# Optimization experiments

Measured on AMD Instinct MI355X. Metric: run time of the kernel, lower is better.

Reference implementation:

```python
import jax, jax.numpy as jnp
from jax import lax
import numpy as np

EPS = 1e-3  # keras BatchNormalization default epsilon

def _bn(x, g, b, m, v):
    return (x - m) / jnp.sqrt(v + EPS) * g + b

def _conv_relu(x, w, b):
    y = lax.conv_general_dilated(x, w, (1, 1), 'SAME', dimension_numbers=('NHWC', 'HWIO', 'NHWC'))
    return jax.nn.relu(y + b)

def _pool(x):
    return lax.reduce_window(x, -jnp.inf, lax.max, (1, 2, 2, 1), (1, 2, 2, 1), 'VALID')

def setup_inputs():
    key = jax.random.key(0)
    ks = jax.random.split(key, 24)
    B, E = 2048, 16
    rn = lambda k, s, sc=0.05: jax.random.normal(k, s, jnp.float32) * sc
    pos = lambda k, s: jax.random.uniform(k, s, jnp.float32, 0.5, 1.5)
    inp = {}
    inp['x'] = jax.random.normal(ks[0], (B, 32, 32, 3), jnp.float32)
    inp['cW1'] = rn(ks[1], (3, 3, 3, 32), 0.2); inp['cb1'] = jnp.zeros((32,), jnp.float32)
    inp['bn1g'] = pos(ks[2], (32,)); inp['bn1b'] = rn(ks[3], (32,))
    inp['bn1m'] = rn(ks[4], (32,)); inp['bn1v'] = pos(ks[5], (32,))
    inp['cW2'] = rn(ks[6], (3, 3, 32, 64), 0.1); inp['cb2'] = jnp.zeros((64,), jnp.float32)
    inp['bn2g'] = pos(ks[7], (64,)); inp['bn2b'] = rn(ks[8], (64,))
    inp['bn2m'] = rn(ks[9], (64,)); inp['bn2v'] = pos(ks[10], (64,))
    inp['dW'] = rn(ks[11], (4096, 128), 0.02); inp['db'] = jnp.zeros((128,), jnp.float32)
    inp['rW1'] = rn(ks[12], (128, 64), 0.1); inp['rb1'] = jnp.zeros((64,), jnp.float32)
    inp['rW2'] = rn(ks[13], (64, E), 0.1); inp['rb2'] = jnp.zeros((E,), jnp.float32)
    inp['eW1'] = rn(ks[14], (E, 128, 128), 0.1); inp['eb1'] = jnp.zeros((E, 128), jnp.float32)
    inp['ebng'] = pos(ks[15], (E, 128)); inp['ebnb'] = rn(ks[16], (E, 128))
    inp['ebnm'] = rn(ks[17], (E, 128)); inp['ebnv'] = pos(ks[18], (E, 128))
    inp['eW2'] = rn(ks[19], (E, 128, 64), 0.1); inp['eb2'] = jnp.zeros((E, 64), jnp.float32)
    inp['eW3'] = rn(ks[20], (E, 64, 10), 0.1); inp['eb3'] = jnp.zeros((E, 10), jnp.float32)
    return inp

def reference(x, cW1, cb1, bn1g, bn1b, bn1m, bn1v, cW2, cb2, bn2g, bn2b, bn2m, bn2v,
              dW, db, rW1, rb1, rW2, rb2, eW1, eb1, ebng, ebnb, ebnm, ebnv, eW2, eb2, eW3, eb3):
    # shared trunk: conv(relu) -> BN -> maxpool, twice; flatten; dense(relu). Dropout = identity (inference).
    h = _pool(_bn(_conv_relu(x, cW1, cb1), bn1g, bn1b, bn1m, bn1v))   # [B,16,16,32]
    h = _pool(_bn(_conv_relu(h, cW2, cb2), bn2g, bn2b, bn2m, bn2v))   # [B,8,8,64]
    feats = jax.nn.relu(h.reshape(h.shape[0], -1) @ dW + db)          # [B,128]
    # router softmax over expert logits
    router_logits = jax.nn.relu(feats @ rW1 + rb1) @ rW2 + rb2        # [B,E]
    router_probs = jax.nn.softmax(router_logits, axis=-1)
    # all experts fused into batched GEMMs over stacked weights: [E,B,*]
    e = jax.nn.relu(jnp.einsum('bd,edh->ebh', feats, eW1) + eb1[:, None, :])
    e = _bn(e, ebng[:, None, :], ebnb[:, None, :], ebnm[:, None, :], ebnv[:, None, :])
    e = jax.nn.relu(jnp.einsum('ebh,ehk->ebk', e, eW2) + eb2[:, None, :])
    e = jnp.einsum('ebk,ekc->ebc', e, eW3) + eb3[:, None, :]          # [E,B,10]
    # weighted sum combine: sum_e probs[b,e] * logits[e,b,c]
    return jnp.einsum('ebc,be->bc', e, router_probs)
```

## Files before the change

kernel.cpp:

```cpp
#include <hip/hip_runtime.h>

#define EPS 1e-3f

typedef _Float16 half8 __attribute__((ext_vector_type(8)));
typedef _Float16 half4v __attribute__((ext_vector_type(4)));
typedef float f32x4 __attribute__((ext_vector_type(4)));

__global__ __launch_bounds__(256) void k_wprep_all(
    const float* __restrict__ dW,  _Float16* __restrict__ Wt2,
    const float* __restrict__ eW1, _Float16* __restrict__ eW1t,
    const float* __restrict__ eW2, _Float16* __restrict__ eW2t,
    const float* __restrict__ cW1, _Float16* __restrict__ Wt1,
    const float* __restrict__ cW2, _Float16* __restrict__ Wt,
    const float* __restrict__ eW3, _Float16* __restrict__ eW3p)
{
    __shared__ _Float16 lsbuf[16640];
    int bx = blockIdx.x, tid = threadIdx.x;

    if (bx < 64) {
        auto lt = (_Float16(*)[137])lsbuf;
        int kb = bx * 64;
        int c = tid & 127, r2 = tid >> 7;
#pragma unroll
        for (int it = 0; it < 32; ++it) {
            int r = it * 2 + r2;
            lt[r][c] = (_Float16)dW[(long)(kb + r) * 128 + c];
        }
        __syncthreads();
#pragma unroll
        for (int it = 0; it < 4; ++it) {
            int chunk = it * 256 + tid;
            int n = chunk >> 3, kc = (chunk & 7) * 8;
            half8 v;
#pragma unroll
            for (int j = 0; j < 8; ++j) v[j] = lt[kc + j][n];
            *(half8*)(Wt2 + (long)n * 4096 + kb + kc) = v;
        }
    } else if (bx < 80) {
        auto lt = (_Float16(*)[130])lsbuf;
        int e = bx - 64;
        const float* src = eW1 + (long)e * 16384;
#pragma unroll
        for (int it = 0; it < 64; ++it) {
            int idx = it * 256 + tid;
            lt[idx >> 7][idx & 127] = (_Float16)src[idx];
        }
        __syncthreads();
        _Float16* dst = eW1t + (long)e * 16384;
#pragma unroll
        for (int it = 0; it < 64; ++it) {
            int idx = it * 256 + tid;
            dst[idx] = lt[idx & 127][idx >> 7];
        }
    } else if (bx < 96) {
        auto lt = (_Float16(*)[66])lsbuf;
        int e = bx - 80;
        const float* src = eW2 + (long)e * 8192;
#pragma unroll
        for (int it = 0; it < 32; ++it) {
            int idx = it * 256 + tid;
            lt[idx >> 6][idx & 63] = (_Float16)src[idx];
        }
        __syncthreads();
        _Float16* dst = eW2t + (long)e * 8192;
#pragma unroll
        for (int it = 0; it < 32; ++it) {
            int idx = it * 256 + tid;
            dst[idx] = lt[idx & 127][idx >> 7];
        }
    } else {
        int t = (bx - 96) * 256 + tid;
        if (t < 3072) {
            int k = t & 31, co = (t >> 5) & 31, ky = t >> 10;
            int kx = k >> 2, ci = k & 3;
            float val = (kx < 3 && ci < 3) ? cW1[((ky * 3 + kx) * 3 + ci) * 32 + co] : 0.f;
            Wt1[t] = (_Float16)val;
        } else if (t < 3072 + 18432) {
            int u = t - 3072;
            int co = u & 63;
            int rest = u >> 6;
            int ci = rest & 31, tap = rest >> 5;
            Wt[(tap * 64 + co) * 32 + ci] = (_Float16)cW2[u];
        } else if (t < 3072 + 18432 + 16384) {
            int u = t - 21504;
            int k = u & 63, n = (u >> 6) & 15, e = u >> 10;
            float val = (n < 10) ? eW3[(e * 64 + k) * 10 + n] : 0.f;
            eW3p[(e * 16 + n) * 64 + k] = (_Float16)val;
        }
    }
}

__global__ __launch_bounds__(256) void k_conv12(
    const float* __restrict__ x, const _Float16* __restrict__ Wt1,
    const float* __restrict__ b1, const float* __restrict__ g1,
    const float* __restrict__ bb1, const float* __restrict__ m1,
    const float* __restrict__ v1,
    const _Float16* __restrict__ Wt,
    const float* __restrict__ b2, const float* __restrict__ g2,
    const float* __restrict__ bb2, const float* __restrict__ m2,
    const float* __restrict__ v2,
    _Float16* __restrict__ out)
{
    __shared__ __align__(16) _Float16 As1[34][40][4];
    __shared__ __align__(16) _Float16 As2[18][18][40];
    int tid = threadIdx.x;
    int b = blockIdx.x;
    int w = tid >> 6, l = tid & 63;
    int l15 = l & 15, lq = l >> 4;

    {
        float4 z = make_float4(0.f, 0.f, 0.f, 0.f);
        float4* f1p = (float4*)&As1[0][0][0];
        for (int i = tid; i < 680; i += 256) f1p[i] = z;
        float4* f2p = (float4*)&As2[0][0][0];
        for (int i = tid; i < 1620; i += 256) f2p[i] = z;
    }
    __syncthreads();

    {
        int y = tid >> 3, x0 = (tid & 7) * 4;
        const float* src = x + ((long)b * 1024 + y * 32 + x0) * 3;
        float4 f0 = *(const float4*)(src);
        float4 f1 = *(const float4*)(src + 4);
        float4 f2 = *(const float4*)(src + 8);
        half4v h0 = { (_Float16)f0.x, (_Float16)f0.y, (_Float16)f0.z, (_Float16)0.f };
        half4v h1 = { (_Float16)f0.w, (_Float16)f1.x, (_Float16)f1.y, (_Float16)0.f };
        half4v h2 = { (_Float16)f1.z, (_Float16)f1.w, (_Float16)f2.x, (_Float16)0.f };
        half4v h3 = { (_Float16)f2.y, (_Float16)f2.z, (_Float16)f2.w, (_Float16)0.f };
        *(half4v*)&As1[y + 1][x0 + 1][0] = h0;
        *(half4v*)&As1[y + 1][x0 + 2][0] = h1;
        *(half4v*)&As1[y + 1][x0 + 3][0] = h2;
        *(half4v*)&As1[y + 1][x0 + 4][0] = h3;
    }

    half8 bf1[3][2];
#pragma unroll
    for (int ky = 0; ky < 3; ++ky)
#pragma unroll
        for (int nf = 0; nf < 2; ++nf)
            bf1[ky][nf] = *(const half8*)(Wt1 + (ky * 32 + nf * 16 + l15) * 32 + lq * 8);

    float bv1[2], gg1[2], iv1[2], mm1[2], bbv1[2];
#pragma unroll
    for (int nf = 0; nf < 2; ++nf) {
        int co = nf * 16 + l15;
        bv1[nf] = b1[co]; gg1[nf] = g1[co]; bbv1[nf] = bb1[co]; mm1[nf] = m1[co];
        iv1[nf] = rsqrtf(v1[co] + EPS);
    }
    __syncthreads();

    {
        int y0 = w * 8;
#pragma unroll
        for (int pr = 0; pr < 4; ++pr) {
            int ya = y0 + 2 * pr;
            f32x4 acc[2][2][2];
#pragma unroll
            for (int r = 0; r < 2; ++r)
#pragma unroll
                for (int h = 0; h < 2; ++h)
#pragma unroll
                    for (int nf = 0; nf < 2; ++nf)
                        acc[r][h][nf] = (f32x4){ bv1[nf], bv1[nf], bv1[nf], bv1[nf] };

#pragma unroll
            for (int ky = 0; ky < 3; ++ky)
#pragma unroll
                for (int r = 0; r < 2; ++r)
#pragma unroll
                    for (int h = 0; h < 2; ++h) {
                        const _Float16* ap = &As1[ya + r + ky][h * 16 + l15 + 2 * lq][0];
                        half4v a0 = *(const half4v*)ap;
                        half4v a1 = *(const half4v*)(ap + 4);
                        half8 af = __builtin_shufflevector(a0, a1, 0, 1, 2, 3, 4, 5, 6, 7);
#pragma unroll
                        for (int nf = 0; nf < 2; ++nf)
                            acc[r][h][nf] = __builtin_amdgcn_mfma_f32_16x16x32_f16(
                                af, bf1[ky][nf], acc[r][h][nf], 0, 0, 0);
                    }

            int py = w * 4 + pr;
#pragma unroll
            for (int h = 0; h < 2; ++h)
#pragma unroll
                for (int nf = 0; nf < 2; ++nf) {
                    f32x4 aA = acc[0][h][nf], aB = acc[1][h][nf];
                    float p0 = fmaxf(fmaxf(aA[0], aA[1]), fmaxf(aB[0], aB[1]));
                    float p1 = fmaxf(fmaxf(aA[2], aA[3]), fmaxf(aB[2], aB[3]));
                    p0 = fmaxf(p0, 0.f); p1 = fmaxf(p1, 0.f);
                    p0 = (p0 - mm1[nf]) * iv1[nf] * gg1[nf] + bbv1[nf];
                    p1 = (p1 - mm1[nf]) * iv1[nf] * gg1[nf] + bbv1[nf];
                    int px = h * 8 + lq * 2;
                    int co = nf * 16 + l15;
                    As2[py + 1][px + 1][co] = (_Float16)p0;
                    As2[py + 1][px + 2][co] = (_Float16)p1;
                }
        }
    }
    __syncthreads();

    f32x4 acc2[4][4];
#pragma unroll
    for (int nf = 0; nf < 4; ++nf) {
        float bv = b2[nf * 16 + l15];
#pragma unroll
        for (int mf = 0; mf < 4; ++mf)
            acc2[mf][nf] = (f32x4){ bv, bv, bv, bv };
    }

    int row0 = 4 * w;
#pragma unroll
    for (int tap = 0; tap < 9; ++tap) {
        int ky = tap / 3, kx = tap % 3;
        half8 bf[4];
        const _Float16* wb = Wt + ((long)(tap * 64 + l15)) * 32 + lq * 8;
#pragma unroll
        for (int nf = 0; nf < 4; ++nf)
            bf[nf] = *(const half8*)(wb + (long)nf * 16 * 32);
#pragma unroll
        for (int mf = 0; mf < 4; ++mf) {
            const _Float16* ap = &As2[row0 + mf + ky][l15 + kx][lq * 8];
            half8 af = *(const half8*)ap;
#pragma unroll
            for (int nf = 0; nf < 4; ++nf)
                acc2[mf][nf] = __builtin_amdgcn_mfma_f32_16x16x32_f16(
                    af, bf[nf], acc2[mf][nf], 0, 0, 0);
        }
    }

#pragma unroll
    for (int nf = 0; nf < 4; ++nf) {
        int co = nf * 16 + l15;
        float gg = g2[co], bbv = bb2[co], mm = m2[co];
        float iv = rsqrtf(v2[co] + EPS);
#pragma unroll
        for (int pr = 0; pr < 2; ++pr) {
            int prow = 2 * w + pr;
            f32x4 a0 = acc2[2 * pr][nf];
            f32x4 a1 = acc2[2 * pr + 1][nf];
            float p0 = fmaxf(fmaxf(a0[0], a0[1]), fmaxf(a1[0], a1[1]));
            float p1 = fmaxf(fmaxf(a0[2], a0[3]), fmaxf(a1[2], a1[3]));
            p0 = fmaxf(p0, 0.f);
            p1 = fmaxf(p1, 0.f);
            int ppx = lq * 2;
            long base = (((long)b * 8 + prow) * 8) * 64 + co;
            out[base + (long)(ppx    ) * 64] = (_Float16)((p0 - mm) * iv * gg + bbv);
            out[base + (long)(ppx + 1) * 64] = (_Float16)((p1 - mm) * iv * gg + bbv);
        }
    }
}

__global__ __launch_bounds__(256) void k_dense_mfma(
    const _Float16* __restrict__ h2f, const _Float16* __restrict__ Wt2,
    float* __restrict__ pws)
{
    __shared__ __align__(16) _Float16 As[16][264];
    int tid = threadIdx.x;
    int w = tid >> 6, l = tid & 63;
    int l15 = l & 15, lq = l >> 4;
    int brow = blockIdx.x * 16;
    int kbase = blockIdx.y * 512;
    int n0 = w * 32;

    f32x4 acc[2] = { (f32x4){0.f,0.f,0.f,0.f}, (f32x4){0.f,0.f,0.f,0.f} };

    int srow = tid >> 4, sc = (tid & 15) * 16;
#pragma unroll
    for (int k0 = 0; k0 < 512; k0 += 256) {
        __syncthreads();
        const _Float16* src = h2f + (long)(brow + srow) * 4096 + kbase + k0 + sc;
        half8 v0 = *(const half8*)src;
        half8 v1 = *(const half8*)(src + 8);
        *(half8*)(&As[srow][sc])     = v0;
        *(half8*)(&As[srow][sc + 8]) = v1;
        __syncthreads();
#pragma unroll
        for (int kk = 0; kk < 256; kk += 32) {
            half8 af = *(const half8*)(&As[l15][kk + lq * 8]);
#pragma unroll
            for (int nf = 0; nf < 2; ++nf) {
                half8 bf = *(const half8*)(Wt2 + (long)(n0 + nf * 16 + l15) * 4096
                                           + kbase + k0 + kk + lq * 8);
                acc[nf] = __builtin_amdgcn_mfma_f32_16x16x32_f16(af, bf, acc[nf], 0, 0, 0);
            }
        }
    }

    float* pbase = pws + (long)blockIdx.y * 262144;
#pragma unroll
    for (int nf = 0; nf < 2; ++nf) {
        int n = n0 + nf * 16 + l15;
#pragma unroll
        for (int reg = 0; reg < 4; ++reg) {
            int b = brow + lq * 4 + reg;
            pbase[(long)b * 128 + n] = acc[nf][reg];
        }
    }
}

__global__ __launch_bounds__(256) void k_reduce_router(
    const float* __restrict__ pws, const float* __restrict__ db,
    const float* __restrict__ rW1, const float* __restrict__ rb1,
    const float* __restrict__ rW2, const float* __restrict__ rb2,
    _Float16* __restrict__ featsH, float* __restrict__ probs)
{
    __shared__ float fsm[16][128];
    __shared__ float r1s[16][64];
    int tid = threadIdx.x;
    int brow = blockIdx.x * 16;
    int r = tid >> 4, c0 = (tid & 15) * 8;

    float acc[8];
#pragma unroll
    for (int j = 0; j < 8; ++j) acc[j] = db[c0 + j];
    long base = (long)(brow + r) * 128 + c0;
#pragma unroll
    for (int kc = 0; kc < 8; ++kc) {
        const float4* p = (const float4*)(pws + (long)kc * 262144 + base);
        float4 v0 = p[0], v1 = p[1];
        acc[0] += v0.x; acc[1] += v0.y; acc[2] += v0.z; acc[3] += v0.w;
        acc[4] += v1.x; acc[5] += v1.y; acc[6] += v1.z; acc[7] += v1.w;
    }
    half8 hv;
#pragma unroll
    for (int j = 0; j < 8; ++j) {
        float val = fmaxf(acc[j], 0.f);
        fsm[r][c0 + j] = val;
        hv[j] = (_Float16)val;
    }
    *(half8*)(featsH + base) = hv;
    __syncthreads();

    {
        int h = tid & 63, bg = tid >> 6;
        float a[4];
#pragma unroll
        for (int i = 0; i < 4; ++i) a[i] = rb1[h];
        for (int d = 0; d < 128; ++d) {
            float wgt = rW1[d * 64 + h];
#pragma unroll
            for (int i = 0; i < 4; ++i) a[i] += fsm[bg * 4 + i][d] * wgt;
        }
#pragma unroll
        for (int i = 0; i < 4; ++i) r1s[bg * 4 + i][h] = fmaxf(a[i], 0.f);
    }
    __syncthreads();

    {
        int b = tid >> 4, e = tid & 15;
        float a = rb2[e];
#pragma unroll 8
        for (int k = 0; k < 64; ++k) a += r1s[b][k] * rW2[k * 16 + e];
        float mx = a;
#pragma unroll
        for (int off = 1; off < 16; off <<= 1)
            mx = fmaxf(mx, __shfl_xor(mx, off, 16));
        float ex = __expf(a - mx);
        float s = ex;
#pragma unroll
        for (int off = 1; off < 16; off <<= 1)
            s += __shfl_xor(s, off, 16);
        probs[(long)(brow + b) * 16 + e] = ex / s;
    }
}

__global__ __launch_bounds__(256) void k_expert_mfma(
    const _Float16* __restrict__ featsH,
    const _Float16* __restrict__ eW1t, const float* __restrict__ eb1,
    const float* __restrict__ g,  const float* __restrict__ bb,
    const float* __restrict__ m,  const float* __restrict__ v,
    const _Float16* __restrict__ eW2t, const float* __restrict__ eb2,
    const _Float16* __restrict__ eW3p, const float* __restrict__ eb3,
    float* __restrict__ e3p)
{
    __shared__ __align__(16) _Float16 fsH[64][136];
    __shared__ __align__(16) _Float16 h1sH[64][136];
    __shared__ __align__(16) _Float16 h2sH[64][72];
    int e = blockIdx.x, bt = blockIdx.y;
    int tid = threadIdx.x;
    int w = tid >> 6, l = tid & 63, l15 = l & 15, lq = l >> 4;
    int brow = bt * 64, m0 = w * 16;

#pragma unroll
    for (int it = 0; it < 4; ++it) {
        int idx = it * 256 + tid;
        int r = idx >> 4, c = (idx & 15) * 8;
        *(half8*)&fsH[r][c] = *(const half8*)(featsH + (long)(brow + r) * 128 + c);
    }
    __syncthreads();

    {
        half8 af[4];
#pragma unroll
        for (int kq = 0; kq < 4; ++kq)
            af[kq] = *(const half8*)&fsH[m0 + l15][kq * 32 + lq * 8];
        const _Float16* B1 = eW1t + (long)e * 16384 + l15 * 128 + lq * 8;
        f32x4 acc[8];
#pragma unroll
        for (int nf = 0; nf < 8; ++nf) {
            float bv = eb1[e * 128 + nf * 16 + l15];
            acc[nf] = (f32x4){ bv, bv, bv, bv };
        }
#pragma unroll
        for (int nf = 0; nf < 8; ++nf)
#pragma unroll
            for (int kq = 0; kq < 4; ++kq) {
                half8 bfv = *(const half8*)(B1 + nf * 2048 + kq * 32);
                acc[nf] = __builtin_amdgcn_mfma_f32_16x16x32_f16(af[kq], bfv, acc[nf], 0, 0, 0);
            }
#pragma unroll
        for (int nf = 0; nf < 8; ++nf) {
            int h = nf * 16 + l15;
            float gg = g[e * 128 + h], bbv = bb[e * 128 + h], mm = m[e * 128 + h];
            float iv = rsqrtf(v[e * 128 + h] + EPS);
#pragma unroll
            for (int reg = 0; reg < 4; ++reg) {
                float val = fmaxf(acc[nf][reg], 0.f);
                h1sH[m0 + lq * 4 + reg][h] = (_Float16)((val - mm) * iv * gg + bbv);
            }
        }
    }
    __syncthreads();

    {
        half8 af[4];
#pragma unroll
        for (int kq = 0; kq < 4; ++kq)
            af[kq] = *(const half8*)&h1sH[m0 + l15][kq * 32 + lq * 8];
        const _Float16* B2 = eW2t + (long)e * 8192 + l15 * 128 + lq * 8;
        f32x4 acc[4];
#pragma unroll
        for (int nf = 0; nf < 4; ++nf) {
            float bv = eb2[e * 64 + nf * 16 + l15];
            acc[nf] = (f32x4){ bv, bv, bv, bv };
        }
#pragma unroll
        for (int nf = 0; nf < 4; ++nf)
#pragma unroll
            for (int kq = 0; kq < 4; ++kq) {
                half8 bfv = *(const half8*)(B2 + nf * 2048 + kq * 32);
                acc[nf] = __builtin_amdgcn_mfma_f32_16x16x32_f16(af[kq], bfv, acc[nf], 0, 0, 0);
            }
#pragma unroll
        for (int nf = 0; nf < 4; ++nf)
#pragma unroll
            for (int reg = 0; reg < 4; ++reg)
                h2sH[m0 + lq * 4 + reg][nf * 16 + l15] = (_Float16)fmaxf(acc[nf][reg], 0.f);
    }
    __syncthreads();

    {
        half8 af[2];
#pragma unroll
        for (int kq = 0; kq < 2; ++kq)
            af[kq] = *(const half8*)&h2sH[m0 + l15][kq * 32 + lq * 8];
        const _Float16* B3 = eW3p + (long)e * 1024 + l15 * 64 + lq * 8;
        float bv = (l15 < 10) ? eb3[e * 10 + l15] : 0.f;
        f32x4 acc = (f32x4){ bv, bv, bv, bv };
#pragma unroll
        for (int kq = 0; kq < 2; ++kq) {
            half8 bfv = *(const half8*)(B3 + kq * 32);
            acc = __builtin_amdgcn_mfma_f32_16x16x32_f16(af[kq], bfv, acc, 0, 0, 0);
        }
#pragma unroll
        for (int reg = 0; reg < 4; ++reg) {
            int b = brow + m0 + lq * 4 + reg;
            e3p[((long)e * 2048 + b) * 16 + l15] = acc[reg];
        }
    }
}

__global__ __launch_bounds__(256) void k_combine(
    const float* __restrict__ e3p, const float* __restrict__ probs,
    float* __restrict__ out)
{
    int t = blockIdx.x * blockDim.x + threadIdx.x;
    if (t >= 2048 * 10) return;
    int b = t / 10, c = t % 10;
    float acc = 0.f;
#pragma unroll
    for (int e = 0; e < 16; ++e)
        acc += probs[(long)b * 16 + e] * e3p[((long)e * 2048 + b) * 16 + c];
    out[t] = acc;
}

extern "C" void kernel_launch(void* const* d_in, const int* in_sizes, int n_in,
                              void* d_out, int out_size, void* d_ws, size_t ws_size,
                              hipStream_t stream)
{
    const float* x    = (const float*)d_in[0];
    const float* cW1  = (const float*)d_in[1];
    const float* cb1  = (const float*)d_in[2];
    const float* bn1g = (const float*)d_in[3];
    const float* bn1b = (const float*)d_in[4];
    const float* bn1m = (const float*)d_in[5];
    const float* bn1v = (const float*)d_in[6];
    const float* cW2  = (const float*)d_in[7];
    const float* cb2  = (const float*)d_in[8];
    const float* bn2g = (const float*)d_in[9];
    const float* bn2b = (const float*)d_in[10];
    const float* bn2m = (const float*)d_in[11];
    const float* bn2v = (const float*)d_in[12];
    const float* dW   = (const float*)d_in[13];
    const float* db   = (const float*)d_in[14];
    const float* rW1  = (const float*)d_in[15];
    const float* rb1  = (const float*)d_in[16];
    const float* rW2  = (const float*)d_in[17];
    const float* rb2  = (const float*)d_in[18];
    const float* eW1  = (const float*)d_in[19];
    const float* eb1  = (const float*)d_in[20];
    const float* ebng = (const float*)d_in[21];
    const float* ebnb = (const float*)d_in[22];
    const float* ebnm = (const float*)d_in[23];
    const float* ebnv = (const float*)d_in[24];
    const float* eW2  = (const float*)d_in[25];
    const float* eb2  = (const float*)d_in[26];
    const float* eW3  = (const float*)d_in[27];
    const float* eb3  = (const float*)d_in[28];

    float* ws    = (float*)d_ws;
    float* h1reg = ws;
    float* e3p   = h1reg;
    _Float16* featsH = (_Float16*)(h1reg + 524288);
    float* h2reg = h1reg + 16777216;
    _Float16* h2f = (_Float16*)h2reg;
    _Float16* Wt2 = (_Float16*)(h2reg + 4194304);
    float* probs = h2reg + 8388608;
    float* ewreg = probs + 32768;
    _Float16* eW1t = (_Float16*)ewreg;
    _Float16* eW2t = eW1t + 262144;
    _Float16* eW3p = eW2t + 131072;
    _Float16* Wt   = eW3p + 16384;
    _Float16* Wt1  = Wt + 18432;
    float* pws   = ewreg + 262144;
    float* out   = (float*)d_out;

    k_wprep_all<<<244, 256, 0, stream>>>(dW, Wt2, eW1, eW1t, eW2, eW2t,
                                         cW1, Wt1, cW2, Wt, eW3, eW3p);
    k_conv12<<<2048, 256, 0, stream>>>(x, Wt1, cb1, bn1g, bn1b, bn1m, bn1v,
                                       Wt, cb2, bn2g, bn2b, bn2m, bn2v, h2f);
    {
        dim3 grid(128, 8);
        k_dense_mfma<<<grid, 256, 0, stream>>>(h2f, Wt2, pws);
    }
    k_reduce_router<<<128, 256, 0, stream>>>(pws, db, rW1, rb1, rW2, rb2,
                                             featsH, probs);
    {
        dim3 grid(16, 32);
        k_expert_mfma<<<grid, 256, 0, stream>>>(featsH, eW1t, eb1, ebng, ebnb, ebnm, ebnv,
                                                eW2t, eb2, eW3p, eb3, e3p);
    }
    k_combine<<<80, 256, 0, stream>>>(e3p, probs, out);
}
```

Before: 88.10 us.

## Pack two conv1 kernel rows per MFMA K-slice, prefetch conv2 weights, fold BN

```diff
diff --git a/kernel.cpp b/kernel.cpp
--- a/kernel.cpp
+++ b/kernel.cpp
@@ -70,18 +70,20 @@
         }
     } else {
         int t = (bx - 96) * 256 + tid;
-        if (t < 3072) {
-            int k = t & 31, co = (t >> 5) & 31, ky = t >> 10;
-            int kx = k >> 2, ci = k & 3;
-            float val = (kx < 3 && ci < 3) ? cW1[((ky * 3 + kx) * 3 + ci) * 32 + co] : 0.f;
+        if (t < 2048) {
+            int k = t & 31, co = (t >> 5) & 31, p = t >> 10;
+            int kyin = (k >> 4) & 1, kxp = (k >> 2) & 3, ci = k & 3;
+            int ky = 2 * p + kyin;
+            float val = (ky < 3 && kxp < 3 && ci < 3)
+                        ? cW1[((ky * 3 + kxp) * 3 + ci) * 32 + co] : 0.f;
             Wt1[t] = (_Float16)val;
-        } else if (t < 3072 + 18432) {
+        } else if (t >= 3072 && t < 3072 + 18432) {
             int u = t - 3072;
             int co = u & 63;
             int rest = u >> 6;
             int ci = rest & 31, tap = rest >> 5;
             Wt[(tap * 64 + co) * 32 + ci] = (_Float16)cW2[u];
-        } else if (t < 3072 + 18432 + 16384) {
+        } else if (t >= 21504 && t < 21504 + 16384) {
             int u = t - 21504;
             int k = u & 63, n = (u >> 6) & 15, e = u >> 10;
             float val = (n < 10) ? eW3[(e * 64 + k) * 10 + n] : 0.f;
@@ -90,7 +92,7 @@
     }
 }
 
-__global__ __launch_bounds__(256) void k_conv12(
+__global__ __launch_bounds__(256, 4) void k_conv12(
     const float* __restrict__ x, const _Float16* __restrict__ Wt1,
     const float* __restrict__ b1, const float* __restrict__ g1,
     const float* __restrict__ bb1, const float* __restrict__ m1,
@@ -101,17 +103,18 @@
     const float* __restrict__ v2,
     _Float16* __restrict__ out)
 {
-    __shared__ __align__(16) _Float16 As1[34][40][4];
+    __shared__ __align__(16) _Float16 As1[35][40][4];
     __shared__ __align__(16) _Float16 As2[18][18][40];
     int tid = threadIdx.x;
     int b = blockIdx.x;
     int w = tid >> 6, l = tid & 63;
     int l15 = l & 15, lq = l >> 4;
+    int lqr = lq >> 1, lqc = (lq & 1) * 2;
 
     {
         float4 z = make_float4(0.f, 0.f, 0.f, 0.f);
         float4* f1p = (float4*)&As1[0][0][0];
-        for (int i = tid; i < 680; i += 256) f1p[i] = z;
+        for (int i = tid; i < 700; i += 256) f1p[i] = z;
         float4* f2p = (float4*)&As2[0][0][0];
         for (int i = tid; i < 1620; i += 256) f2p[i] = z;
     }
@@ -133,19 +136,21 @@
         *(half4v*)&As1[y + 1][x0 + 4][0] = h3;
     }
 
-    half8 bf1[3][2];
-#pragma unroll
-    for (int ky = 0; ky < 3; ++ky)
+    half8 bf1[2][2];
+#pragma unroll
+    for (int p = 0; p < 2; ++p)
 #pragma unroll
         for (int nf = 0; nf < 2; ++nf)
-            bf1[ky][nf] = *(const half8*)(Wt1 + (ky * 32 + nf * 16 + l15) * 32 + lq * 8);
-
-    float bv1[2], gg1[2], iv1[2], mm1[2], bbv1[2];
+            bf1[p][nf] = *(const half8*)(Wt1 + (p * 32 + nf * 16 + l15) * 32 + lq * 8);
+
+    float bv1[2], S1[2], T1[2];
 #pragma unroll
     for (int nf = 0; nf < 2; ++nf) {
         int co = nf * 16 + l15;
-        bv1[nf] = b1[co]; gg1[nf] = g1[co]; bbv1[nf] = bb1[co]; mm1[nf] = m1[co];
-        iv1[nf] = rsqrtf(v1[co] + EPS);
+        bv1[nf] = b1[co];
+        float s = rsqrtf(v1[co] + EPS) * g1[co];
+        S1[nf] = s;
+        T1[nf] = bb1[co] - m1[co] * s;
     }
     __syncthreads();
 
@@ -164,19 +169,19 @@
                         acc[r][h][nf] = (f32x4){ bv1[nf], bv1[nf], bv1[nf], bv1[nf] };
 
 #pragma unroll
-            for (int ky = 0; ky < 3; ++ky)
+            for (int p = 0; p < 2; ++p)
 #pragma unroll
                 for (int r = 0; r < 2; ++r)
 #pragma unroll
                     for (int h = 0; h < 2; ++h) {
-                        const _Float16* ap = &As1[ya + r + ky][h * 16 + l15 + 2 * lq][0];
+                        const _Float16* ap = &As1[ya + r + 2 * p + lqr][h * 16 + l15 + lqc][0];
                         half4v a0 = *(const half4v*)ap;
                         half4v a1 = *(const half4v*)(ap + 4);
                         half8 af = __builtin_shufflevector(a0, a1, 0, 1, 2, 3, 4, 5, 6, 7);
 #pragma unroll
                         for (int nf = 0; nf < 2; ++nf)
                             acc[r][h][nf] = __builtin_amdgcn_mfma_f32_16x16x32_f16(
-                                af, bf1[ky][nf], acc[r][h][nf], 0, 0, 0);
+                                af, bf1[p][nf], acc[r][h][nf], 0, 0, 0);
                     }
 
             int py = w * 4 + pr;
@@ -188,8 +193,8 @@
                     float p0 = fmaxf(fmaxf(aA[0], aA[1]), fmaxf(aB[0], aB[1]));
                     float p1 = fmaxf(fmaxf(aA[2], aA[3]), fmaxf(aB[2], aB[3]));
                     p0 = fmaxf(p0, 0.f); p1 = fmaxf(p1, 0.f);
-                    p0 = (p0 - mm1[nf]) * iv1[nf] * gg1[nf] + bbv1[nf];
-                    p1 = (p1 - mm1[nf]) * iv1[nf] * gg1[nf] + bbv1[nf];
+                    p0 = fmaf(p0, S1[nf], T1[nf]);
+                    p1 = fmaf(p1, S1[nf], T1[nf]);
                     int px = h * 8 + lq * 2;
                     int co = nf * 16 + l15;
                     As2[py + 1][px + 1][co] = (_Float16)p0;
@@ -209,14 +214,23 @@
     }
 
     int row0 = 4 * w;
+    half8 bfc[2][4];
+    {
+        const _Float16* wb = Wt + ((long)l15) * 32 + lq * 8;
+#pragma unroll
+        for (int nf = 0; nf < 4; ++nf)
+            bfc[0][nf] = *(const half8*)(wb + (long)nf * 16 * 32);
+    }
 #pragma unroll
     for (int tap = 0; tap < 9; ++tap) {
+        int cur = tap & 1, nxt = cur ^ 1;
+        if (tap < 8) {
+            const _Float16* wb = Wt + ((long)((tap + 1) * 64 + l15)) * 32 + lq * 8;
+#pragma unroll
+            for (int nf = 0; nf < 4; ++nf)
+                bfc[nxt][nf] = *(const half8*)(wb + (long)nf * 16 * 32);
+        }
         int ky = tap / 3, kx = tap % 3;
-        half8 bf[4];
-        const _Float16* wb = Wt + ((long)(tap * 64 + l15)) * 32 + lq * 8;
-#pragma unroll
-        for (int nf = 0; nf < 4; ++nf)
-            bf[nf] = *(const half8*)(wb + (long)nf * 16 * 32);
 #pragma unroll
         for (int mf = 0; mf < 4; ++mf) {
             const _Float16* ap = &As2[row0 + mf + ky][l15 + kx][lq * 8];
@@ -224,15 +238,15 @@
 #pragma unroll
             for (int nf = 0; nf < 4; ++nf)
                 acc2[mf][nf] = __builtin_amdgcn_mfma_f32_16x16x32_f16(
-                    af, bf[nf], acc2[mf][nf], 0, 0, 0);
+                    af, bfc[cur][nf], acc2[mf][nf], 0, 0, 0);
         }
     }
 
 #pragma unroll
     for (int nf = 0; nf < 4; ++nf) {
         int co = nf * 16 + l15;
-        float gg = g2[co], bbv = bb2[co], mm = m2[co];
-        float iv = rsqrtf(v2[co] + EPS);
+        float s = rsqrtf(v2[co] + EPS) * g2[co];
+        float t2 = bb2[co] - m2[co] * s;
 #pragma unroll
         for (int pr = 0; pr < 2; ++pr) {
             int prow = 2 * w + pr;
@@ -244,8 +258,8 @@
             p1 = fmaxf(p1, 0.f);
             int ppx = lq * 2;
             long base = (((long)b * 8 + prow) * 8) * 64 + co;
-            out[base + (long)(ppx    ) * 64] = (_Float16)((p0 - mm) * iv * gg + bbv);
-            out[base + (long)(ppx + 1) * 64] = (_Float16)((p1 - mm) * iv * gg + bbv);
+            out[base + (long)(ppx    ) * 64] = (_Float16)fmaf(p0, s, t2);
+            out[base + (long)(ppx + 1) * 64] = (_Float16)fmaf(p1, s, t2);
         }
     }
 }
```

Result: slower. 92.49 us (+5.0%).
